# Kernel tuning notes

Hardware: AMD Instinct MI355X
Metric: run time of the kernel (lower is better)

Reference implementation:

```python
import jax, jax.numpy as jnp
import numpy as np

LABELS = (1, 2, 3)  # from init_kwargs
EPS = float(np.finfo(np.float32).eps)
SHAPE = (512, 512, 512)


def setup_inputs() -> dict:
    key = jax.random.key(0)
    k1, k2 = jax.random.split(key)
    # label maps with values in {0,1,2,3}, stored as float32 (equality-compared)
    vol1 = jax.random.randint(k1, SHAPE, 0, 4).astype(jnp.float32)
    vol2 = jax.random.randint(k2, SHAPE, 0, 4).astype(jnp.float32)
    return {"vol1": vol1, "vol2": vol2}


def reference(vol1, vol2):
    # Per-label Dice: dice_l = 2*|A_l & B_l| / (|A_l| + |B_l| + eps)
    dices = []
    for lab in LABELS:  # fixed tiny label set -> loop is fine
        labv = jnp.asarray(lab, dtype=vol1.dtype)
        m1 = vol1 == labv
        m2 = vol2 == labv
        top = 2.0 * jnp.sum(m1 & m2).astype(jnp.float32)
        bottom = jnp.sum(m1).astype(jnp.float32) + jnp.sum(m2).astype(jnp.float32)
        dices.append(top / (bottom + EPS))
    dicem = jnp.stack(dices)
    return 1.0 - jnp.mean(dicem)
```

## Files before the change

kernel.cpp:

```cpp
#include <hip/hip_runtime.h>


#define NCNT 9

__global__ void dice_zero_ws(unsigned int* counters) {
    int i = threadIdx.x;
    if (i < NCNT) counters[i] = 0u;
}

__global__ __launch_bounds__(256) void dice_count(const float4* __restrict__ a,
                                                  const float4* __restrict__ b,
                                                  unsigned int* __restrict__ counters,
                                                  int n4) {
    unsigned int c[NCNT];
#pragma unroll
    for (int k = 0; k < NCNT; ++k) c[k] = 0u;

    const int stride = gridDim.x * blockDim.x;
    for (int i = blockIdx.x * blockDim.x + threadIdx.x; i < n4; i += stride) {
        float4 x = a[i];
        float4 y = b[i];
#pragma unroll
        for (int comp = 0; comp < 4; ++comp) {
            float xa = (comp == 0) ? x.x : (comp == 1) ? x.y : (comp == 2) ? x.z : x.w;
            float yb = (comp == 0) ? y.x : (comp == 1) ? y.y : (comp == 2) ? y.z : y.w;
            bool a1 = (xa == 1.0f), a2 = (xa == 2.0f), a3 = (xa == 3.0f);
            bool b1 = (yb == 1.0f), b2 = (yb == 2.0f), b3 = (yb == 3.0f);
            c[0] += a1; c[1] += a2; c[2] += a3;
            c[3] += b1; c[4] += b2; c[5] += b3;
            c[6] += a1 & b1; c[7] += a2 & b2; c[8] += a3 & b3;
        }
    }

#pragma unroll
    for (int k = 0; k < NCNT; ++k) {
#pragma unroll
        for (int off = 32; off > 0; off >>= 1)
            c[k] += __shfl_down(c[k], off, 64);
    }

    __shared__ unsigned int s[4][NCNT];
    const int wave = threadIdx.x >> 6;
    const int lane = threadIdx.x & 63;
    if (lane == 0) {
#pragma unroll
        for (int k = 0; k < NCNT; ++k) s[wave][k] = c[k];
    }
    __syncthreads();
    if (threadIdx.x == 0) {
#pragma unroll
        for (int k = 0; k < NCNT; ++k) {
            unsigned int v = s[0][k] + s[1][k] + s[2][k] + s[3][k];
            atomicAdd(&counters[k], v);
        }
    }
}

__global__ void dice_finalize(const unsigned int* __restrict__ counters,
                              float* __restrict__ out) {
    const double eps = 1.1920928955078125e-07;
    double acc = 0.0;
#pragma unroll
    for (int l = 0; l < 3; ++l) {
        double c1 = (double)counters[l];
        double c2 = (double)counters[3 + l];
        double in = (double)counters[6 + l];
        acc += (2.0 * in) / (c1 + c2 + eps);
    }
    out[0] = (float)(1.0 - acc / 3.0);
}

extern "C" void kernel_launch(void* const* d_in, const int* in_sizes, int n_in,
                              void* d_out, int out_size, void* d_ws, size_t ws_size,
                              hipStream_t stream) {
    const float* v1 = (const float*)d_in[0];
    const float* v2 = (const float*)d_in[1];
    float* out = (float*)d_out;
    unsigned int* counters = (unsigned int*)d_ws;

    const int n = in_sizes[0];
    const int n4 = n >> 2;

    dice_zero_ws<<<1, 64, 0, stream>>>(counters);

    const int threads = 256;
    const int blocks = 2048;
    dice_count<<<blocks, threads, 0, stream>>>(
        (const float4*)v1, (const float4*)v2, counters, n4);

    dice_finalize<<<1, 1, 0, stream>>>(counters, out);
}
```

Before: 1.128 ms.

## Stream inputs via global_load_lds and replace atomics with per-block partials

```diff
diff --git a/kernel.cpp b/kernel.cpp
--- a/kernel.cpp
+++ b/kernel.cpp
@@ -1,31 +1,82 @@
 #include <hip/hip_runtime.h>
+#include <stdint.h>
 
 
 #define NCNT 9
+#define NBLK 2048
+#define TPB  256
 
-__global__ void dice_zero_ws(unsigned int* counters) {
-    int i = threadIdx.x;
-    if (i < NCNT) counters[i] = 0u;
+typedef unsigned int v4u __attribute__((ext_vector_type(4)));
+typedef __attribute__((address_space(3))) uint8_t lds8_t;
+typedef __attribute__((address_space(1))) const uint8_t glb8_t;
+
+#define F1 0x3F800000u
+#define F2 0x40000000u
+#define F3 0x40400000u
+
+__device__ __forceinline__ void count4u(v4u x, v4u y, unsigned int* c) {
+#pragma unroll
+    for (int comp = 0; comp < 4; ++comp) {
+        const unsigned v = x[comp];
+        const unsigned w = y[comp];
+        bool a1 = (v == F1), a2 = (v == F2), a3 = (v == F3);
+        bool b1 = (w == F1), b2 = (w == F2), b3 = (w == F3);
+        c[0] += a1; c[1] += a2; c[2] += a3;
+        c[3] += b1; c[4] += b2; c[5] += b3;
+        c[6] += a1 & b1; c[7] += a2 & b2; c[8] += a3 & b3;
+    }
 }
 
-__global__ __launch_bounds__(256) void dice_count(const float4* __restrict__ a,
-                                                  const float4* __restrict__ b,
-                                                  unsigned int* __restrict__ counters,
-                                                  int n4) {
+__global__ __launch_bounds__(TPB, 8) void dice_count(const uint8_t* __restrict__ a,
+                                                     const uint8_t* __restrict__ b,
+                                                     unsigned int* __restrict__ partials,
+                                                     long long n_bytes) {
+    __shared__ uint8_t smem[16384];
+
     unsigned int c[NCNT];
 #pragma unroll
     for (int k = 0; k < NCNT; ++k) c[k] = 0u;
 
-    const int stride = gridDim.x * blockDim.x;
-    for (int i = blockIdx.x * blockDim.x + threadIdx.x; i < n4; i += stride) {
-        float4 x = a[i];
-        float4 y = b[i];
-#pragma unroll
-        for (int comp = 0; comp < 4; ++comp) {
-            float xa = (comp == 0) ? x.x : (comp == 1) ? x.y : (comp == 2) ? x.z : x.w;
-            float yb = (comp == 0) ? y.x : (comp == 1) ? y.y : (comp == 2) ? y.z : y.w;
-            bool a1 = (xa == 1.0f), a2 = (xa == 2.0f), a3 = (xa == 3.0f);
-            bool b1 = (yb == 1.0f), b2 = (yb == 2.0f), b3 = (yb == 3.0f);
+    const int w = threadIdx.x >> 6;
+    const int l = threadIdx.x & 63;
+
+    const long long block_bytes = 8192;
+    const long long gstride = (long long)gridDim.x * block_bytes;
+    const int iters = (int)(n_bytes / gstride);
+
+    lds8_t* la = (lds8_t*)&smem[w * 2048];
+    lds8_t* lb = (lds8_t*)&smem[8192 + w * 2048];
+    const v4u* ra = (const v4u*)&smem[w * 2048 + l * 16];
+    const v4u* rb = (const v4u*)&smem[8192 + w * 2048 + l * 16];
+
+    for (int j = 0; j < iters; ++j) {
+        const long long base = (long long)j * gstride
+                             + (long long)blockIdx.x * block_bytes
+                             + (long long)w * 2048 + (long long)l * 16;
+        __builtin_amdgcn_global_load_lds((glb8_t*)(a + base),        la,        16, 0, 0);
+        __builtin_amdgcn_global_load_lds((glb8_t*)(a + base + 1024), la + 1024, 16, 0, 0);
+        __builtin_amdgcn_global_load_lds((glb8_t*)(b + base),        lb,        16, 0, 0);
+        __builtin_amdgcn_global_load_lds((glb8_t*)(b + base + 1024), lb + 1024, 16, 0, 0);
+        __builtin_amdgcn_sched_barrier(0);
+        __builtin_amdgcn_s_waitcnt(0xF70);
+        __builtin_amdgcn_sched_barrier(0);
+        v4u xa0 = ra[0], xa1 = ra[64];
+        v4u yb0 = rb[0], yb1 = rb[64];
+        count4u(xa0, yb0, c);
+        count4u(xa1, yb1, c);
+    }
+
+    {
+        const long long done = (long long)iters * gstride;
+        const unsigned int* au = (const unsigned int*)a;
+        const unsigned int* bu = (const unsigned int*)b;
+        const long long n_elem = n_bytes >> 2;
+        for (long long e = (done >> 2) + blockIdx.x * TPB + threadIdx.x;
+             e < n_elem; e += (long long)gridDim.x * TPB) {
+            const unsigned v = au[e];
+            const unsigned ww = bu[e];
+            bool a1 = (v == F1), a2 = (v == F2), a3 = (v == F3);
+            bool b1 = (ww == F1), b2 = (ww == F2), b3 = (ww == F3);
             c[0] += a1; c[1] += a2; c[2] += a3;
             c[3] += b1; c[4] += b2; c[5] += b3;
             c[6] += a1 & b1; c[7] += a2 & b2; c[8] += a3 & b3;
@@ -39,54 +90,69 @@
             c[k] += __shfl_down(c[k], off, 64);
     }
 
-    __shared__ unsigned int s[4][NCNT];
-    const int wave = threadIdx.x >> 6;
-    const int lane = threadIdx.x & 63;
-    if (lane == 0) {
+    __syncthreads();
+    unsigned int* s = (unsigned int*)smem;
+    if (l == 0) {
 #pragma unroll
-        for (int k = 0; k < NCNT; ++k) s[wave][k] = c[k];
+        for (int k = 0; k < NCNT; ++k) s[w * NCNT + k] = c[k];
     }
     __syncthreads();
     if (threadIdx.x == 0) {
 #pragma unroll
         for (int k = 0; k < NCNT; ++k) {
-            unsigned int v = s[0][k] + s[1][k] + s[2][k] + s[3][k];
-            atomicAdd(&counters[k], v);
+            partials[blockIdx.x * NCNT + k] =
+                s[0 * NCNT + k] + s[1 * NCNT + k] + s[2 * NCNT + k] + s[3 * NCNT + k];
         }
     }
 }
 
-__global__ void dice_finalize(const unsigned int* __restrict__ counters,
-                              float* __restrict__ out) {
-    const double eps = 1.1920928955078125e-07;
-    double acc = 0.0;
+__global__ __launch_bounds__(TPB) void dice_finalize(const unsigned int* __restrict__ partials,
+                                                     float* __restrict__ out, int nblk) {
+    unsigned int c[NCNT];
 #pragma unroll
-    for (int l = 0; l < 3; ++l) {
-        double c1 = (double)counters[l];
-        double c2 = (double)counters[3 + l];
-        double in = (double)counters[6 + l];
-        acc += (2.0 * in) / (c1 + c2 + eps);
+    for (int k = 0; k < NCNT; ++k) c[k] = 0u;
+    for (int bidx = threadIdx.x; bidx < nblk; bidx += TPB) {
+#pragma unroll
+        for (int k = 0; k < NCNT; ++k) c[k] += partials[bidx * NCNT + k];
     }
-    out[0] = (float)(1.0 - acc / 3.0);
+#pragma unroll
+    for (int k = 0; k < NCNT; ++k) {
+#pragma unroll
+        for (int off = 32; off > 0; off >>= 1)
+            c[k] += __shfl_down(c[k], off, 64);
+    }
+    __shared__ unsigned int s[4][NCNT];
+    const int w = threadIdx.x >> 6;
+    const int l = threadIdx.x & 63;
+    if (l == 0) {
+#pragma unroll
+        for (int k = 0; k < NCNT; ++k) s[w][k] = c[k];
+    }
+    __syncthreads();
+    if (threadIdx.x == 0) {
+        const double eps = 1.1920928955078125e-07;
+        double acc = 0.0;
+#pragma unroll
+        for (int lab = 0; lab < 3; ++lab) {
+            double c1 = (double)(s[0][lab] + s[1][lab] + s[2][lab] + s[3][lab]);
+            double c2 = (double)(s[0][3 + lab] + s[1][3 + lab] + s[2][3 + lab] + s[3][3 + lab]);
+            double in = (double)(s[0][6 + lab] + s[1][6 + lab] + s[2][6 + lab] + s[3][6 + lab]);
+            acc += (2.0 * in) / (c1 + c2 + eps);
+        }
+        out[0] = (float)(1.0 - acc / 3.0);
+    }
 }
 
 extern "C" void kernel_launch(void* const* d_in, const int* in_sizes, int n_in,
                               void* d_out, int out_size, void* d_ws, size_t ws_size,
                               hipStream_t stream) {
-    const float* v1 = (const float*)d_in[0];
-    const float* v2 = (const float*)d_in[1];
+    const uint8_t* v1 = (const uint8_t*)d_in[0];
+    const uint8_t* v2 = (const uint8_t*)d_in[1];
     float* out = (float*)d_out;
-    unsigned int* counters = (unsigned int*)d_ws;
+    unsigned int* partials = (unsigned int*)d_ws;
 
-    const int n = in_sizes[0];
-    const int n4 = n >> 2;
+    const long long n_bytes = (long long)in_sizes[0] * 4;
 
-    dice_zero_ws<<<1, 64, 0, stream>>>(counters);
-
-    const int threads = 256;
-    const int blocks = 2048;
-    dice_count<<<blocks, threads, 0, stream>>>(
-        (const float4*)v1, (const float4*)v2, counters, n4);
-
-    dice_finalize<<<1, 1, 0, stream>>>(counters, out);
+    dice_count<<<NBLK, TPB, 0, stream>>>(v1, v2, partials, n_bytes);
+    dice_finalize<<<1, TPB, 0, stream>>>(partials, out, NBLK);
 }
```

Result: faster. 969.7 us (-14.1%).
